# Kernel tuning notes

Hardware: AMD Instinct MI355X
Metric: run time of the kernel (lower is better)

Reference implementation:

```python
import jax, jax.numpy as jnp
import numpy as np

DIM = 64
POS_H = 64
ATTN_H = 4 * DIM
B, N = 2, 512


def setup_inputs() -> dict:
    key = jax.random.key(0)
    ks = jax.random.split(key, 20)
    g = lambda k, shape, fan_in: jax.random.normal(k, shape, jnp.float32) / np.sqrt(fan_in)
    return {
        "x": jax.random.normal(ks[0], (B, N, DIM), jnp.float32),
        "pos": jax.random.normal(ks[1], (B, N, 3), jnp.float32),
        "prev_w": g(ks[2], (DIM, DIM), DIM), "prev_b": jnp.zeros((DIM,), jnp.float32),
        "q_w": g(ks[3], (DIM, DIM), DIM),
        "k_w": g(ks[4], (DIM, DIM), DIM),
        "v_w": g(ks[5], (DIM, DIM), DIM),
        "pos_w1": g(ks[6], (3, POS_H), 3), "pos_b1": jnp.zeros((POS_H,), jnp.float32),
        "pos_w2": g(ks[7], (POS_H, DIM), POS_H), "pos_b2": jnp.zeros((DIM,), jnp.float32),
        "attn_w1": g(ks[8], (DIM, ATTN_H), DIM), "attn_b1": jnp.zeros((ATTN_H,), jnp.float32),
        "attn_w2": g(ks[9], (ATTN_H, DIM), ATTN_H), "attn_b2": jnp.zeros((DIM,), jnp.float32),
        "fin_w": g(ks[10], (DIM, DIM), DIM), "fin_b": jnp.zeros((DIM,), jnp.float32),
    }


def reference(x, pos, prev_w, prev_b, q_w, k_w, v_w,
              pos_w1, pos_b1, pos_w2, pos_b2,
              attn_w1, attn_b1, attn_w2, attn_b2, fin_w, fin_b):
    # prev_linear
    x1 = x @ prev_w + prev_b                              # [B,N,D]
    q = x1 @ q_w                                          # [B,N,D]
    k = x1 @ k_w
    v = x1 @ v_w
    # relative position embedding: [B,i,j,3] -> MLP -> [B,i,j,D]
    rel_pos = pos[:, :, None, :] - pos[:, None, :, :]
    rpe = jax.nn.relu(rel_pos @ pos_w1 + pos_b1) @ pos_w2 + pos_b2
    # per-pair qk difference + attn MLP -> vector (channel-wise) attention logits
    qk_rel = q[:, :, None, :] - k[:, None, :, :]          # [B,i,j,D]
    sim = jax.nn.relu((qk_rel + rpe) @ attn_w1 + attn_b1) @ attn_w2 + attn_b2  # [B,i,j,D]
    # v indexed by j, plus pairwise positional embedding
    v2 = v[:, None, :, :] + rpe                           # [B,i,j,D]
    attn = jax.nn.softmax(sim, axis=2)                    # softmax over j (dim=-2 of [B,i,j,D])
    agg = jnp.einsum('bijd,bijd->bid', attn, v2)          # [B,N,D]
    x_out = agg @ fin_w + fin_b + x1                      # final_linear + residual
    return (x_out, pos)
```

## Files before the change

### kernel.cpp

```cpp
#include <hip/hip_runtime.h>

typedef __attribute__((ext_vector_type(4))) float f32x4;
typedef __attribute__((ext_vector_type(8))) __bf16 bf16x8;
typedef __attribute__((ext_vector_type(4))) __bf16 bf16x4;
typedef __attribute__((ext_vector_type(2))) unsigned int u32x2;

template<int OFF>
__device__ __forceinline__ u32x2 tr_read_o(unsigned base){
    u32x2 d;
    asm volatile("ds_read_b64_tr_b16 %0, %1 offset:%c2"
                 : "=v"(d) : "v"(base), "i"(OFF));
    return d;
}
__device__ __forceinline__ bf16x8 frag_cat(u32x2 a, u32x2 b){
    union { u32x2 u[2]; bf16x8 f; } c; c.u[0] = a; c.u[1] = b; return c.f;
}


__global__ void ptb_pre(const float* __restrict__ x,
                        const float* __restrict__ pos,
                        const float* __restrict__ prev_w,
                        const float* __restrict__ prev_b,
                        const float* __restrict__ q_w,
                        const float* __restrict__ k_w,
                        const float* __restrict__ v_w,
                        const float* __restrict__ pos_w2,
                        const float* __restrict__ attn_w1,
                        const float* __restrict__ attn_b1,
                        float* __restrict__ ws,
                        float* __restrict__ out)
{
    const int bid = blockIdx.x;
    const int tid = threadIdx.x;
    __shared__ float xr[256], x1r[256], qsh[256], ksh[256], vsh[256];

    float wcol[64];
    #pragma unroll
    for (int c = 0; c < 64; ++c) wcol[c] = attn_w1[c*256 + tid];

    if (bid >= 256){
        xr[tid] = pos_w2[(bid - 256)*256 + tid];
        __syncthreads();
        float* Wp = ws + 655360;
        #pragma unroll
        for (int r = 0; r < 4; ++r){
            float s = 0.f;
            #pragma unroll 16
            for (int c = 0; c < 64; ++c) s += xr[r*64 + c] * wcol[c];
            Wp[((bid - 256)*4 + r)*256 + tid] = s;
        }
        return;
    }

    const int rr  = tid >> 6, d = tid & 63;
    const int row = bid*4 + rr;
    xr[tid] = x[row*64 + d];
    __syncthreads();
    float a = prev_b[d];
    #pragma unroll 16
    for (int c = 0; c < 64; ++c) a += xr[rr*64 + c] * prev_w[c*64 + d];
    x1r[tid] = a;
    ws[row*64 + d] = a;
    __syncthreads();
    float qv = 0.f, kv = 0.f, vv = 0.f;
    #pragma unroll 16
    for (int c = 0; c < 64; ++c){
        float t = x1r[rr*64 + c];
        qv += t * q_w[c*64 + d];
        kv += t * k_w[c*64 + d];
        vv += t * v_w[c*64 + d];
    }
    qsh[tid] = qv; ksh[tid] = kv; vsh[tid] = vv;
    if (tid < 12) out[65536 + bid*12 + tid] = pos[bid*12 + tid];
    __syncthreads();

    ws[65536 + bid*256 + tid] = vsh[(tid & 3)*64 + (tid >> 2)];

    float* Q1  = ws + 131072;
    float* K1s = ws + 393216;
    const float bb = attn_b1[tid];
    float sq[4], sk[4];
    #pragma unroll
    for (int r = 0; r < 4; ++r){ sq[r] = bb; sk[r] = 0.f; }
    #pragma unroll 16
    for (int c = 0; c < 64; ++c){
        const float wv = wcol[c];
        #pragma unroll
        for (int r = 0; r < 4; ++r){
            sq[r] += qsh[r*64 + c] * wv;
            sk[r] += ksh[r*64 + c] * wv;
        }
    }
    #pragma unroll
    for (int r = 0; r < 4; ++r) Q1[(bid*4 + r)*256 + tid] = sq[r];
    f32x4 kvec = {sk[0], sk[1], sk[2], sk[3]};
    *(f32x4*)&K1s[bid*1024 + tid*4] = kvec;
}

__global__ __launch_bounds__(256) void ptb_main(
    const float* __restrict__ pos,
    const float* __restrict__ pos_w1, const float* __restrict__ pos_b1,
    const float* __restrict__ pos_w2, const float* __restrict__ pos_b2,
    const float* __restrict__ attn_w2, const float* __restrict__ attn_b2,
    const float* __restrict__ fin_w, const float* __restrict__ fin_b,
    const float* __restrict__ ws, float* __restrict__ out)
{
    const int blk = blockIdx.x;
    const int b   = blk >> 9;
    const int i   = blk & 511;
    const int tid = threadIdx.x;
    const int w   = tid >> 6;
    const int l   = tid & 63;
    const int lg  = l >> 4;
    const int ln  = l & 15;

    __shared__ __bf16 sH1[2][64][64];
    __shared__ __align__(16) char sHT[18432];
    __shared__ float sPW1[192], sPB1[64], sAGG[64], sPOSI[3];

    const float* x1p = ws;
    const float* vs  = ws + 65536;
    const float* Q1  = ws + 131072;
    const float* K1s = ws + 393216;
    const float* Wp  = ws + 655360;

    if (tid < 64) sPB1[tid] = pos_b1[tid];
    if (tid >= 64 && tid < 256) sPW1[tid - 64] = pos_w1[tid - 64];
    if (tid < 3) sPOSI[tid] = pos[(b*512 + i)*3 + tid];

    const int dch  = w*16 + ln;
    const int Ew   = w*64;
    const int swzA = (ln & 7) << 3;

    bf16x8 w1f[2][4];
    #pragma unroll
    for (int kf = 0; kf < 2; ++kf)
        #pragma unroll
        for (int et = 0; et < 4; ++et)
            #pragma unroll
            for (int ii = 0; ii < 8; ++ii)
                w1f[kf][et][ii] = (__bf16)Wp[(kf*32 + lg*8 + ii)*256 + Ew + et*16 + ln];
    bf16x8 w2f[8];
    #pragma unroll
    for (int kf = 0; kf < 8; ++kf)
        #pragma unroll
        for (int ii = 0; ii < 8; ++ii)
            w2f[kf][ii] = (__bf16)attn_w2[(kf*32 + lg*8 + ii)*64 + dch];
    bf16x8 pwfw[2];
    #pragma unroll
    for (int kf = 0; kf < 2; ++kf)
        #pragma unroll
        for (int ii = 0; ii < 8; ++ii)
            pwfw[kf][ii] = (__bf16)pos_w2[(kf*32 + lg*8 + ii)*64 + dch];

    float Q1b[4];
    #pragma unroll
    for (int et = 0; et < 4; ++et) Q1b[et] = Q1[blk*256 + Ew + et*16 + ln];
    const float pb2v = pos_b2[dch];
    const float b2v  = attn_b2[dch];

    const unsigned sHTb = (unsigned)(unsigned long long)&sHT[0];
    const unsigned trbase = sHTb + (unsigned)(lg*288 + ln*8);

    float mrun = -1e30f, srun = 0.f, arun = 0.f;

    auto stageA = [&](int j0a){
        const int bufa = (j0a >> 6) & 1;
        const float* pj = &pos[(b*512 + j0a + w*16 + ln)*3];
        const float r0 = sPOSI[0] - pj[0];
        const float r1 = sPOSI[1] - pj[1];
        const float r2 = sPOSI[2] - pj[2];
        #pragma unroll
        for (int kf = 0; kf < 2; ++kf){
            const int hb = kf*32 + lg*8;
            f32x4 wa0 = *(const f32x4*)&sPW1[      hb],   wa1 = *(const f32x4*)&sPW1[      hb+4];
            f32x4 wb0 = *(const f32x4*)&sPW1[ 64 + hb],   wb1 = *(const f32x4*)&sPW1[ 64 + hb+4];
            f32x4 wc0 = *(const f32x4*)&sPW1[128 + hb],   wc1 = *(const f32x4*)&sPW1[128 + hb+4];
            f32x4 bb0 = *(const f32x4*)&sPB1[      hb],   bb1 = *(const f32x4*)&sPB1[      hb+4];
            bf16x8 h1f;
            #pragma unroll
            for (int ii = 0; ii < 4; ++ii){
                float hv0 = bb0[ii] + r0*wa0[ii] + r1*wb0[ii] + r2*wc0[ii];
                float hv1 = bb1[ii] + r0*wa1[ii] + r1*wb1[ii] + r2*wc1[ii];
                h1f[ii]   = (__bf16)fmaxf(hv0, 0.f);
                h1f[ii+4] = (__bf16)fmaxf(hv1, 0.f);
            }
            *(bf16x8*)&sH1[bufa][w*16 + ln][hb ^ swzA] = h1f;
        }
    };

    __syncthreads();
    stageA(0);

    #pragma unroll 1
    for (int t = 0; t < 8; ++t){
        const int j0  = t << 6;
        const int buf = t & 1;
        __syncthreads();
        if (t < 7) stageA(j0 + 64);
        #pragma unroll 1
        for (int hb = 0; hb < 2; ++hb){
            f32x4 rcs[2];
            #pragma unroll
            for (int jj = 0; jj < 2; ++jj){
                const int jrow = hb*32 + jj*16;
                const int krow = ((b*512 + j0 + jrow) >> 2) + lg;
                const bf16x8 af0 = *(const bf16x8*)&sH1[buf][jrow + ln][(     lg*8) ^ swzA];
                const bf16x8 af1 = *(const bf16x8*)&sH1[buf][jrow + ln][(32 + lg*8) ^ swzA];
                f32x4 accs[4];
                #pragma unroll
                for (int et = 0; et < 4; ++et){
                    const f32x4 kw4 = *(const f32x4*)&K1s[krow*1024 + (Ew + et*16 + ln)*4];
                    const f32x4 qv4 = {Q1b[et], Q1b[et], Q1b[et], Q1b[et]};
                    accs[et] = qv4 - kw4;
                }
                __builtin_amdgcn_s_setprio(1);
                #pragma unroll
                for (int et = 0; et < 4; ++et)
                    accs[et] = __builtin_amdgcn_mfma_f32_16x16x32_bf16(af0, w1f[0][et], accs[et], 0, 0, 0);
                #pragma unroll
                for (int et = 0; et < 4; ++et)
                    accs[et] = __builtin_amdgcn_mfma_f32_16x16x32_bf16(af1, w1f[1][et], accs[et], 0, 0, 0);
                f32x4 rcv = {pb2v, pb2v, pb2v, pb2v};
                rcv = __builtin_amdgcn_mfma_f32_16x16x32_bf16(af0, pwfw[0], rcv, 0, 0, 0);
                rcv = __builtin_amdgcn_mfma_f32_16x16x32_bf16(af1, pwfw[1], rcv, 0, 0, 0);
                rcs[jj] = rcv;
                __builtin_amdgcn_s_setprio(0);
                #pragma unroll
                for (int et = 0; et < 4; ++et){
                    bf16x4 hp;
                    #pragma unroll
                    for (int ri = 0; ri < 4; ++ri) hp[ri] = (__bf16)fmaxf(accs[et][ri], 0.f);
                    *(bf16x4*)(sHT + (jj*64 + w*16 + et*4 + (ln>>2))*144
                                   + (ln&3)*32 + lg*8) = hp;
                }
            }
            __syncthreads();
            f32x4 accv[2], vvv[2];
            #pragma unroll
            for (int jj = 0; jj < 2; ++jj){
                const int vrow = ((b*512 + j0 + hb*32 + jj*16) >> 2) + lg;
                vvv[jj] = *(const f32x4*)&vs[vrow*256 + dch*4];
            }
            #pragma unroll
            for (int jj = 0; jj < 2; ++jj){
                const unsigned trb = trbase + (unsigned)(jj*9216);
                u32x2 hh[16];
                #define TR2(KF) \
                    hh[(KF)*2]   = tr_read_o<(KF)*1152      >(trb); \
                    hh[(KF)*2+1] = tr_read_o<(KF)*1152 + 144>(trb);
                TR2(0) TR2(1) TR2(2) TR2(3) TR2(4) TR2(5) TR2(6) TR2(7)
                #undef TR2
                asm volatile("s_waitcnt lgkmcnt(8)" ::: "memory");
                __builtin_amdgcn_sched_barrier(0);
                f32x4 a0 = {b2v, b2v, b2v, b2v};
                f32x4 a1 = {0.f, 0.f, 0.f, 0.f};
                __builtin_amdgcn_s_setprio(1);
                a0 = __builtin_amdgcn_mfma_f32_16x16x32_bf16(frag_cat(hh[0], hh[1]), w2f[0], a0, 0, 0, 0);
                a1 = __builtin_amdgcn_mfma_f32_16x16x32_bf16(frag_cat(hh[2], hh[3]), w2f[1], a1, 0, 0, 0);
                a0 = __builtin_amdgcn_mfma_f32_16x16x32_bf16(frag_cat(hh[4], hh[5]), w2f[2], a0, 0, 0, 0);
                a1 = __builtin_amdgcn_mfma_f32_16x16x32_bf16(frag_cat(hh[6], hh[7]), w2f[3], a1, 0, 0, 0);
                __builtin_amdgcn_s_setprio(0);
                asm volatile("s_waitcnt lgkmcnt(0)" ::: "memory");
                __builtin_amdgcn_sched_barrier(0);
                __builtin_amdgcn_s_setprio(1);
                a0 = __builtin_amdgcn_mfma_f32_16x16x32_bf16(frag_cat(hh[8],  hh[9]),  w2f[4], a0, 0, 0, 0);
                a1 = __builtin_amdgcn_mfma_f32_16x16x32_bf16(frag_cat(hh[10], hh[11]), w2f[5], a1, 0, 0, 0);
                a0 = __builtin_amdgcn_mfma_f32_16x16x32_bf16(frag_cat(hh[12], hh[13]), w2f[6], a0, 0, 0, 0);
                a1 = __builtin_amdgcn_mfma_f32_16x16x32_bf16(frag_cat(hh[14], hh[15]), w2f[7], a1, 0, 0, 0);
                __builtin_amdgcn_s_setprio(0);
                accv[jj] = a0 + a1;
            }
            float tmax = fmaxf(fmaxf(fmaxf(accv[0][0], accv[0][1]),
                                     fmaxf(accv[0][2], accv[0][3])),
                               fmaxf(fmaxf(accv[1][0], accv[1][1]),
                                     fmaxf(accv[1][2], accv[1][3])));
            tmax = fmaxf(tmax, __shfl_xor(tmax, 16));
            tmax = fmaxf(tmax, __shfl_xor(tmax, 32));
            const float mnew  = fmaxf(mrun, tmax);
            const float scale = __expf(mrun - mnew);
            srun *= scale; arun *= scale; mrun = mnew;
            #pragma unroll
            for (int jj = 0; jj < 2; ++jj)
                #pragma unroll
                for (int ri = 0; ri < 4; ++ri){
                    const float p = __expf(accv[jj][ri] - mnew);
                    srun += p;
                    arun += p * (vvv[jj][ri] + rcs[jj][ri]);
                }
            if (hb == 0) __syncthreads();
        }
    }

    arun += __shfl_xor(arun, 16); arun += __shfl_xor(arun, 32);
    srun += __shfl_xor(srun, 16); srun += __shfl_xor(srun, 32);
    if (lg == 0) sAGG[dch] = arun / srun;
    __syncthreads();

    if (tid < 64){
        float a = fin_b[tid] + x1p[blk*64 + tid];
        #pragma unroll 16
        for (int c = 0; c < 64; ++c) a += sAGG[c] * fin_w[c*64 + tid];
        out[blk*64 + tid] = a;
    }
}

extern "C" void kernel_launch(void* const* d_in, const int* in_sizes, int n_in,
                              void* d_out, int out_size, void* d_ws, size_t ws_size,
                              hipStream_t stream)
{
    const float* x       = (const float*)d_in[0];
    const float* pos     = (const float*)d_in[1];
    const float* prev_w  = (const float*)d_in[2];
    const float* prev_b  = (const float*)d_in[3];
    const float* q_w     = (const float*)d_in[4];
    const float* k_w     = (const float*)d_in[5];
    const float* v_w     = (const float*)d_in[6];
    const float* pos_w1  = (const float*)d_in[7];
    const float* pos_b1  = (const float*)d_in[8];
    const float* pos_w2  = (const float*)d_in[9];
    const float* pos_b2  = (const float*)d_in[10];
    const float* attn_w1 = (const float*)d_in[11];
    const float* attn_b1 = (const float*)d_in[12];
    const float* attn_w2 = (const float*)d_in[13];
    const float* attn_b2 = (const float*)d_in[14];
    const float* fin_w   = (const float*)d_in[15];
    const float* fin_b   = (const float*)d_in[16];
    float* out = (float*)d_out;
    float* ws  = (float*)d_ws;

    ptb_pre<<<272, 256, 0, stream>>>(x, pos, prev_w, prev_b, q_w, k_w, v_w,
                                     pos_w2, attn_w1, attn_b1, ws, out);
    ptb_main<<<1024, 256, 0, stream>>>(pos, pos_w1, pos_b1, pos_w2, pos_b2,
                                       attn_w2, attn_b2, fin_w, fin_b, ws, out);
}
```

Baseline: 106.7 us.

## Split j range across two blocks per row with partial softmax merge kernel

Each query row is now processed by two blocks, each covering half of the j range, and each writes a partial running max, sum and weighted accumulator to the workspace. A new small kernel merges the two partials and applies the final linear layer plus residual. The position-MLP stage is also changed from a double-buffered shared array to computing into registers and committing to a single buffer late in the iteration, which reduces LDS use. The intent is more blocks for better occupancy and latency hiding. The cost is an extra launch, partial-result traffic, and duplicated weight-fragment loading per block.

Result: slower. 109.9 us (+3.1%).

```diff
diff --git a/kernel.cpp b/kernel.cpp
--- a/kernel.cpp
+++ b/kernel.cpp
@@ -102,23 +102,23 @@
     const float* __restrict__ pos_w1, const float* __restrict__ pos_b1,
     const float* __restrict__ pos_w2, const float* __restrict__ pos_b2,
     const float* __restrict__ attn_w2, const float* __restrict__ attn_b2,
-    const float* __restrict__ fin_w, const float* __restrict__ fin_b,
-    const float* __restrict__ ws, float* __restrict__ out)
+    const float* __restrict__ ws, float* __restrict__ wsp)
 {
     const int blk = blockIdx.x;
-    const int b   = blk >> 9;
-    const int i   = blk & 511;
+    const int ib  = blk >> 1;
+    const int jh  = blk & 1;
+    const int b   = ib >> 9;
+    const int i   = ib & 511;
     const int tid = threadIdx.x;
     const int w   = tid >> 6;
     const int l   = tid & 63;
     const int lg  = l >> 4;
     const int ln  = l & 15;
 
-    __shared__ __bf16 sH1[2][64][64];
+    __shared__ __bf16 sH1[64][64];
     __shared__ __align__(16) char sHT[18432];
-    __shared__ float sPW1[192], sPB1[64], sAGG[64], sPOSI[3];
-
-    const float* x1p = ws;
+    __shared__ float sPW1[192], sPB1[64], sPOSI[3];
+
     const float* vs  = ws + 65536;
     const float* Q1  = ws + 131072;
     const float* K1s = ws + 393216;
@@ -155,7 +155,7 @@
 
     float Q1b[4];
     #pragma unroll
-    for (int et = 0; et < 4; ++et) Q1b[et] = Q1[blk*256 + Ew + et*16 + ln];
+    for (int et = 0; et < 4; ++et) Q1b[et] = Q1[ib*256 + Ew + et*16 + ln];
     const float pb2v = pos_b2[dch];
     const float b2v  = attn_b2[dch];
 
@@ -164,12 +164,13 @@
 
     float mrun = -1e30f, srun = 0.f, arun = 0.f;
 
-    auto stageA = [&](int j0a){
-        const int bufa = (j0a >> 6) & 1;
+    bf16x8 h1r0, h1r1;
+    auto computeA = [&](int j0a){
         const float* pj = &pos[(b*512 + j0a + w*16 + ln)*3];
         const float r0 = sPOSI[0] - pj[0];
         const float r1 = sPOSI[1] - pj[1];
         const float r2 = sPOSI[2] - pj[2];
+        bf16x8 o[2];
         #pragma unroll
         for (int kf = 0; kf < 2; ++kf){
             const int hb = kf*32 + lg*8;
@@ -177,27 +178,31 @@
             f32x4 wb0 = *(const f32x4*)&sPW1[ 64 + hb],   wb1 = *(const f32x4*)&sPW1[ 64 + hb+4];
             f32x4 wc0 = *(const f32x4*)&sPW1[128 + hb],   wc1 = *(const f32x4*)&sPW1[128 + hb+4];
             f32x4 bb0 = *(const f32x4*)&sPB1[      hb],   bb1 = *(const f32x4*)&sPB1[      hb+4];
-            bf16x8 h1f;
             #pragma unroll
             for (int ii = 0; ii < 4; ++ii){
                 float hv0 = bb0[ii] + r0*wa0[ii] + r1*wb0[ii] + r2*wc0[ii];
                 float hv1 = bb1[ii] + r0*wa1[ii] + r1*wb1[ii] + r2*wc1[ii];
-                h1f[ii]   = (__bf16)fmaxf(hv0, 0.f);
-                h1f[ii+4] = (__bf16)fmaxf(hv1, 0.f);
+                o[kf][ii]   = (__bf16)fmaxf(hv0, 0.f);
+                o[kf][ii+4] = (__bf16)fmaxf(hv1, 0.f);
             }
-            *(bf16x8*)&sH1[bufa][w*16 + ln][hb ^ swzA] = h1f;
         }
+        h1r0 = o[0]; h1r1 = o[1];
     };
-
-    __syncthreads();
-    stageA(0);
+    auto commitA = [&](){
+        *(bf16x8*)&sH1[w*16 + ln][(     lg*8) ^ swzA] = h1r0;
+        *(bf16x8*)&sH1[w*16 + ln][(32 + lg*8) ^ swzA] = h1r1;
+    };
+
+    const int t0 = jh*4;
+    __syncthreads();
+    computeA(t0 << 6);
+    commitA();
 
     #pragma unroll 1
-    for (int t = 0; t < 8; ++t){
-        const int j0  = t << 6;
-        const int buf = t & 1;
+    for (int t = t0; t < t0 + 4; ++t){
+        const int j0 = t << 6;
         __syncthreads();
-        if (t < 7) stageA(j0 + 64);
+        if (t < t0 + 3) computeA(j0 + 64);
         #pragma unroll 1
         for (int hb = 0; hb < 2; ++hb){
             f32x4 rcs[2];
@@ -205,8 +210,8 @@
             for (int jj = 0; jj < 2; ++jj){
                 const int jrow = hb*32 + jj*16;
                 const int krow = ((b*512 + j0 + jrow) >> 2) + lg;
-                const bf16x8 af0 = *(const bf16x8*)&sH1[buf][jrow + ln][(     lg*8) ^ swzA];
-                const bf16x8 af1 = *(const bf16x8*)&sH1[buf][jrow + ln][(32 + lg*8) ^ swzA];
+                const bf16x8 af0 = *(const bf16x8*)&sH1[jrow + ln][(     lg*8) ^ swzA];
+                const bf16x8 af1 = *(const bf16x8*)&sH1[jrow + ln][(32 + lg*8) ^ swzA];
                 f32x4 accs[4];
                 #pragma unroll
                 for (int et = 0; et < 4; ++et){
@@ -236,6 +241,7 @@
                 }
             }
             __syncthreads();
+            if (hb == 1 && t < t0 + 3) commitA();
             f32x4 accv[2], vvv[2];
             #pragma unroll
             for (int jj = 0; jj < 2; ++jj){
@@ -294,15 +300,34 @@
 
     arun += __shfl_xor(arun, 16); arun += __shfl_xor(arun, 32);
     srun += __shfl_xor(srun, 16); srun += __shfl_xor(srun, 32);
-    if (lg == 0) sAGG[dch] = arun / srun;
-    __syncthreads();
-
-    if (tid < 64){
-        float a = fin_b[tid] + x1p[blk*64 + tid];
-        #pragma unroll 16
-        for (int c = 0; c < 64; ++c) a += sAGG[c] * fin_w[c*64 + tid];
-        out[blk*64 + tid] = a;
-    }
+    if (lg == 0){
+        float* P = wsp + 671744 + blk*192;
+        P[dch]       = mrun;
+        P[64 + dch]  = srun;
+        P[128 + dch] = arun;
+    }
+}
+
+__global__ void ptb_fin(const float* __restrict__ fin_w,
+                        const float* __restrict__ fin_b,
+                        const float* __restrict__ ws,
+                        float* __restrict__ out)
+{
+    const int ib  = blockIdx.x;
+    const int tid = threadIdx.x;
+    const float* P0 = ws + 671744 + (ib*2    )*192;
+    const float* P1 = ws + 671744 + (ib*2 + 1)*192;
+    __shared__ float sAGG[64];
+    const float m0 = P0[tid], s0 = P0[64+tid], a0 = P0[128+tid];
+    const float m1 = P1[tid], s1 = P1[64+tid], a1 = P1[128+tid];
+    const float M  = fmaxf(m0, m1);
+    const float e0 = __expf(m0 - M), e1 = __expf(m1 - M);
+    sAGG[tid] = (a0*e0 + a1*e1) / (s0*e0 + s1*e1);
+    __syncthreads();
+    float a = fin_b[tid] + ws[ib*64 + tid];
+    #pragma unroll 16
+    for (int c = 0; c < 64; ++c) a += sAGG[c] * fin_w[c*64 + tid];
+    out[ib*64 + tid] = a;
 }
 
 extern "C" void kernel_launch(void* const* d_in, const int* in_sizes, int n_in,
@@ -331,6 +356,7 @@
 
     ptb_pre<<<272, 256, 0, stream>>>(x, pos, prev_w, prev_b, q_w, k_w, v_w,
                                      pos_w2, attn_w1, attn_b1, ws, out);
-    ptb_main<<<1024, 256, 0, stream>>>(pos, pos_w1, pos_b1, pos_w2, pos_b2,
-                                       attn_w2, attn_b2, fin_w, fin_b, ws, out);
-}
+    ptb_main<<<2048, 256, 0, stream>>>(pos, pos_w1, pos_b1, pos_w2, pos_b2,
+                                       attn_w2, attn_b2, ws, ws);
+    ptb_fin<<<1024, 64, 0, stream>>>(fin_w, fin_b, ws, out);
+}
```
